# Kernel tuning notes

Measured on AMD Instinct MI355X. Metric: run time of the kernel, lower is better.

Reference implementation:

```python
import jax, jax.numpy as jnp
import numpy as np

C = 256
HEADS = 8
HD = C // HEADS
SCALE = HD ** -0.5


def conv1x1(x, W, b):
    # x: [B,C_in,H,W], W: [C_out,C_in], b: [C_out]
    return jnp.einsum('oc,bchw->bohw', W, x) + b[None, :, None, None]


def setup_inputs() -> dict:
    key = jax.random.key(0)
    ks = jax.random.split(key, 12)
    B, H, Wd = 2, 48, 48
    s = C ** -0.5
    return {
        'x': jax.random.normal(ks[0], (B, C, H, Wd), jnp.float32),
        'uncertainty': jax.random.uniform(ks[1], (B, 1, H, Wd), jnp.float32),
        'Wq': jax.random.normal(ks[2], (C, C), jnp.float32) * s,
        'bq': jnp.zeros((C,), jnp.float32),
        'Wk': jax.random.normal(ks[3], (C, C), jnp.float32) * s,
        'bk': jnp.zeros((C,), jnp.float32),
        'Wv': jax.random.normal(ks[4], (C, C), jnp.float32) * s,
        'bv': jnp.zeros((C,), jnp.float32),
        'Wg': jax.random.normal(ks[5], (C, 1), jnp.float32),
        'bg': jnp.zeros((C,), jnp.float32),
        'Wo': jax.random.normal(ks[6], (C, C), jnp.float32) * s,
        'bo': jnp.zeros((C,), jnp.float32),
    }


def reference(x, uncertainty, Wq, bq, Wk, bk, Wv, bv, Wg, bg, Wo, bo):
    B, _, H, Wd = x.shape
    N = H * Wd
    # uncertainty gate (1x1 conv from 1 channel to C channels)
    uw = conv1x1(uncertainty, Wg, bg)            # [B,C,H,W]
    gated_x = x * (1.0 - uw)
    q = conv1x1(gated_x, Wq, bq).reshape(B, HEADS, HD, N)
    k = conv1x1(gated_x, Wk, bk).reshape(B, HEADS, HD, N)
    v = conv1x1(x, Wv, bv).reshape(B, HEADS, HD, N)
    # scores: [B,h,N,N] (query tokens n, key tokens m)
    scores = jnp.einsum('bhdn,bhdm->bhnm', q, k) * SCALE
    u_flat = uncertainty.reshape(B, 1, 1, N)      # mask over key axis
    scores = scores * (1.0 - u_flat)
    attn = jax.nn.softmax(scores, axis=-1)
    out = jnp.einsum('bhnm,bhdm->bhdn', attn, v)  # [B,h,hd,N]
    out = out.reshape(B, C, H, Wd)
    out = conv1x1(out, Wo, bo)
    return out + x
```

## Files before the change

### kernel.cpp

```cpp
#include <hip/hip_runtime.h>
#include <hip/hip_bf16.h>

typedef float f32x4 __attribute__((ext_vector_type(4)));
typedef __bf16 bf16x8 __attribute__((ext_vector_type(8)));
typedef __bf16 bf16x4 __attribute__((ext_vector_type(4)));
typedef short s16x4 __attribute__((ext_vector_type(4)));

constexpr int C = 256;
constexpr int N = 2304;
constexpr int T = 2 * N;

#if __has_builtin(__builtin_amdgcn_exp2f)
#define EXP2F(x) __builtin_amdgcn_exp2f(x)
#else
#define EXP2F(x) exp2f(x)
#endif

__device__ __forceinline__ bf16x8 load_bf8(const __bf16* p) {
    return *reinterpret_cast<const bf16x8*>(p);
}

__device__ __forceinline__ f32x4 mfma32(bf16x8 a, bf16x8 b, f32x4 c) {
    return __builtin_amdgcn_mfma_f32_16x16x32_bf16(a, b, c, 0, 0, 0);
}

#if __has_builtin(__builtin_amdgcn_mfma_f32_16x16x16bf16_1k)
__device__ __forceinline__ f32x4 mfma16(bf16x4 a, bf16x4 b, f32x4 c) {
    return __builtin_amdgcn_mfma_f32_16x16x16bf16_1k(
        __builtin_bit_cast(s16x4, a), __builtin_bit_cast(s16x4, b), c, 0, 0, 0);
}
#else
__device__ __forceinline__ f32x4 mfma16(bf16x4 a, bf16x4 b, f32x4 c) {
    f32x4 d;
    asm volatile("v_mfma_f32_16x16x16_bf16 %0, %1, %2, %3"
                 : "=v"(d) : "v"(a), "v"(b), "v"(c));
    return d;
}
#endif

__device__ __forceinline__ void gload_lds16(const __bf16* g, __bf16* l) {
    __builtin_amdgcn_global_load_lds(
        (const __attribute__((address_space(1))) void*)g,
        (__attribute__((address_space(3))) void*)l, 16, 0, 0);
}

#define VMCNT2() asm volatile("s_waitcnt vmcnt(2)" ::: "memory")
#define VMCNT0() asm volatile("s_waitcnt vmcnt(0)" ::: "memory")
#define LGKM0()  asm volatile("s_waitcnt lgkmcnt(0)" ::: "memory")

__global__ void wconv_kernel(const float* __restrict__ Wq, const float* __restrict__ Wk,
                             const float* __restrict__ Wv, const float* __restrict__ Wo,
                             __bf16* __restrict__ Wb) {
    const float* srcs[4] = {Wq, Wk, Wv, Wo};
    int m = blockIdx.x >> 6;
    int idx = (blockIdx.x & 63) * 256 + threadIdx.x;
    float4 v = reinterpret_cast<const float4*>(srcs[m])[idx];
    bf16x4 o = { (__bf16)v.x, (__bf16)v.y, (__bf16)v.z, (__bf16)v.w };
    reinterpret_cast<bf16x4*>(Wb + m * 65536)[idx] = o;
}

__global__ void prep_kernel(const float* __restrict__ x, const float* __restrict__ u,
                            const float* __restrict__ Wg, const float* __restrict__ bg,
                            __bf16* __restrict__ xT, __bf16* __restrict__ gxT) {
    __shared__ float tile[64][65];
    int b = blockIdx.z, c0 = blockIdx.y * 64, n0 = blockIdx.x * 64;
    int t = threadIdx.x;
    const float* xp = x + (b * C + c0) * N + n0;
    #pragma unroll
    for (int r = 0; r < 16; ++r) {
        int cl = r * 4 + (t >> 6);
        int nl = t & 63;
        tile[cl][nl] = xp[cl * N + nl];
    }
    __syncthreads();
    int cq = (t & 15) * 4;
    #pragma unroll
    for (int it = 0; it < 4; ++it) {
        int nl = it * 16 + (t >> 4);
        float uv = u[b * N + n0 + nl];
        bf16x4 xo, go;
        #pragma unroll
        for (int j = 0; j < 4; ++j) {
            int c = c0 + cq + j;
            float xv = tile[cq + j][nl];
            float gate = 1.0f - (Wg[c] * uv + bg[c]);
            xo[j] = (__bf16)xv;
            go[j] = (__bf16)(xv * gate);
        }
        int tok = b * N + n0 + nl;
        *reinterpret_cast<bf16x4*>(xT + (long)tok * C + c0 + cq) = xo;
        *reinterpret_cast<bf16x4*>(gxT + (long)tok * C + c0 + cq) = go;
    }
}

__global__ __launch_bounds__(256) void qkv_kernel(const __bf16* __restrict__ Wb,
    const __bf16* __restrict__ xT, const __bf16* __restrict__ gxT,
    const float* __restrict__ bq, const float* __restrict__ bk, const float* __restrict__ bv,
    const float* __restrict__ u,
    __bf16* __restrict__ Q, __bf16* __restrict__ K, __bf16* __restrict__ V) {
    int proj = blockIdx.z;
    int o0 = blockIdx.y * 64;
    int t0 = blockIdx.x * 32;
    int wave = threadIdx.x >> 6, lane = threadIdx.x & 63;
    int g = lane >> 4, r = lane & 15;
    int ow = o0 + wave * 16;
    const __bf16* W = Wb + proj * 65536;
    const __bf16* inp = (proj == 2) ? xT : gxT;
    f32x4 acc[2] = {};
    for (int k = 0; k < 8; ++k) {
        bf16x8 a = load_bf8(W + (ow + r) * C + k * 32 + g * 8);
        #pragma unroll
        for (int tb = 0; tb < 2; ++tb) {
            bf16x8 bfr = load_bf8(inp + (long)(t0 + tb * 16 + r) * C + k * 32 + g * 8);
            acc[tb] = mfma32(a, bfr, acc[tb]);
        }
    }
    const float* bias = (proj == 0) ? bq : (proj == 1) ? bk : bv;
    float bvw[4];
    #pragma unroll
    for (int i = 0; i < 4; ++i) bvw[i] = bias[ow + g * 4 + i];
    int h = ow >> 5, d0 = (ow & 31) + g * 4;
    const float SC = 0.17677669529663687f * 1.4426950408889634f;
    #pragma unroll
    for (int tb = 0; tb < 2; ++tb) {
        int t = t0 + tb * 16 + r;
        int b = t / N, n = t % N;
        if (proj == 2) {
            #pragma unroll
            for (int i = 0; i < 4; ++i)
                V[((long)(b * 8 + h) * 32 + d0 + i) * N + n] = (__bf16)(acc[tb][i] + bvw[i]);
        } else {
            bf16x4 outv;
            if (proj == 1) {
                float scale = SC * (1.0f - u[t]);
                #pragma unroll
                for (int i = 0; i < 4; ++i) outv[i] = (__bf16)((acc[tb][i] + bvw[i]) * scale);
            } else {
                #pragma unroll
                for (int i = 0; i < 4; ++i) outv[i] = (__bf16)(acc[tb][i] + bvw[i]);
            }
            __bf16* dst = (proj == 0) ? Q : K;
            *reinterpret_cast<bf16x4*>(dst + ((long)(b * 8 + h) * N + n) * 32 + d0) = outv;
        }
    }
}

__global__ __launch_bounds__(256) void attn_kernel(const __bf16* __restrict__ Q,
    const __bf16* __restrict__ K, const __bf16* __restrict__ V,
    __bf16* __restrict__ aoT) {
    __shared__ __bf16 sK[2][2048];
    __shared__ __bf16 sV[2][2048];
    int id = blockIdx.x;
    int xcd = id & 7, j = id >> 3;
    int bh = xcd + 8 * (j / 36);
    int qblk = j % 36;
    int wave = threadIdx.x >> 6, lane = threadIdx.x & 63;
    int g = lane >> 4, r = lane & 15;
    int q0w = qblk * 64 + wave * 16;
    const __bf16* Qg = Q + (long)bh * N * 32;
    const __bf16* Kg = K + (long)bh * N * 32;
    const __bf16* Vg = V + (long)bh * 32 * N;
    bf16x8 qf = load_bf8(Qg + (q0w + r) * 32 + g * 8);
    long ksrc = (long)(wave * 64 + lane) * 8;
    int vd = wave * 8 + (lane >> 3);
    long vsrc = (long)vd * N + ((lane & 7) ^ (lane >> 3)) * 8;
    __bf16* sKb = &sK[0][0];
    __bf16* sVb = &sV[0][0];
    int sOff = wave * 512;
    bf16x4 onesv;
    #pragma unroll
    for (int i = 0; i < 4; ++i) onesv[i] = (__bf16)1.0f;
    f32x4 oa0 = {}, oa1 = {}, oal = {};
    gload_lds16(Kg + ksrc, sKb + sOff);
    gload_lds16(Vg + vsrc, sVb + sOff);
    gload_lds16(Kg + 64 * 32 + ksrc, sKb + 2048 + sOff);
    gload_lds16(Vg + vsrc + 64, sVb + 2048 + sOff);
    int vswz = (r & 7) << 3;
    for (int t = 0; t < 36; ++t) {
        if (t < 35) { VMCNT2(); } else { VMCNT0(); }
        __builtin_amdgcn_s_barrier();
        const __bf16* kb = sKb + (t & 1) * 2048;
        const __bf16* vb = sVb + (t & 1) * 2048;
        bf16x8 kc0 = load_bf8(kb + (0 * 16 + r) * 32 + g * 8);
        bf16x8 kc1 = load_bf8(kb + (1 * 16 + r) * 32 + g * 8);
        bf16x8 kc2 = load_bf8(kb + (2 * 16 + r) * 32 + g * 8);
        bf16x8 kc3 = load_bf8(kb + (3 * 16 + r) * 32 + g * 8);
        bf16x4 vf[4][2];
        #pragma unroll
        for (int tt = 0; tt < 4; ++tt)
            #pragma unroll
            for (int dt = 0; dt < 2; ++dt)
                vf[tt][dt] = *reinterpret_cast<const bf16x4*>(
                    vb + (dt * 16 + r) * 64 + ((tt * 16 + g * 4) ^ vswz));
        f32x4 z = {};
        __builtin_amdgcn_s_setprio(1);
        f32x4 s0 = mfma32(kc0, qf, z);
        f32x4 s1 = mfma32(kc1, qf, z);
        f32x4 s2 = mfma32(kc2, qf, z);
        f32x4 s3 = mfma32(kc3, qf, z);
        __builtin_amdgcn_s_setprio(0);
        bf16x4 pa0, pa1, pa2, pa3;
        #pragma unroll
        for (int i = 0; i < 4; ++i) pa0[i] = (__bf16)EXP2F(s0[i]);
        #pragma unroll
        for (int i = 0; i < 4; ++i) pa1[i] = (__bf16)EXP2F(s1[i]);
        #pragma unroll
        for (int i = 0; i < 4; ++i) pa2[i] = (__bf16)EXP2F(s2[i]);
        #pragma unroll
        for (int i = 0; i < 4; ++i) pa3[i] = (__bf16)EXP2F(s3[i]);
        __builtin_amdgcn_s_setprio(1);
        oa0 = mfma16(vf[0][0], pa0, oa0);
        oa1 = mfma16(vf[0][1], pa0, oa1);
        oal = mfma16(onesv,    pa0, oal);
        oa0 = mfma16(vf[1][0], pa1, oa0);
        oa1 = mfma16(vf[1][1], pa1, oa1);
        oal = mfma16(onesv,    pa1, oal);
        oa0 = mfma16(vf[2][0], pa2, oa0);
        oa1 = mfma16(vf[2][1], pa2, oa1);
        oal = mfma16(onesv,    pa2, oal);
        oa0 = mfma16(vf[3][0], pa3, oa0);
        oa1 = mfma16(vf[3][1], pa3, oa1);
        oal = mfma16(onesv,    pa3, oal);
        __builtin_amdgcn_s_setprio(0);
        LGKM0();
        __builtin_amdgcn_s_barrier();
        if (t < 34) {
            long m0n = (long)(t + 2) * 64;
            gload_lds16(Kg + m0n * 32 + ksrc, sKb + (t & 1) * 2048 + sOff);
            gload_lds16(Vg + vsrc + m0n, sVb + (t & 1) * 2048 + sOff);
        }
    }
    float inv = 1.0f / oal[0];
    int b = bh >> 3, h = bh & 7;
    long tok = (long)b * N + q0w + r;
    bf16x4 ov0, ov1;
    #pragma unroll
    for (int i = 0; i < 4; ++i) ov0[i] = (__bf16)(oa0[i] * inv);
    #pragma unroll
    for (int i = 0; i < 4; ++i) ov1[i] = (__bf16)(oa1[i] * inv);
    *reinterpret_cast<bf16x4*>(aoT + tok * C + h * 32 + g * 4) = ov0;
    *reinterpret_cast<bf16x4*>(aoT + tok * C + h * 32 + 16 + g * 4) = ov1;
}

__global__ __launch_bounds__(256) void outp_kernel(const __bf16* __restrict__ Wb,
    const __bf16* __restrict__ aoT, const float* __restrict__ bo,
    const float* __restrict__ x, float* __restrict__ out) {
    int o0 = blockIdx.y * 64;
    int t0 = blockIdx.x * 32;
    int wave = threadIdx.x >> 6, lane = threadIdx.x & 63;
    int g = lane >> 4, r = lane & 15;
    int ow = o0 + wave * 16;
    const __bf16* W = Wb + 3 * 65536;
    f32x4 acc[2] = {};
    for (int k = 0; k < 8; ++k) {
        bf16x8 a = load_bf8(W + (ow + r) * C + k * 32 + g * 8);
        #pragma unroll
        for (int tb = 0; tb < 2; ++tb) {
            bf16x8 bfr = load_bf8(aoT + (long)(t0 + tb * 16 + r) * C + k * 32 + g * 8);
            acc[tb] = mfma32(a, bfr, acc[tb]);
        }
    }
    float bvw[4];
    #pragma unroll
    for (int i = 0; i < 4; ++i) bvw[i] = bo[ow + g * 4 + i];
    #pragma unroll
    for (int tb = 0; tb < 2; ++tb) {
        int t = t0 + tb * 16 + r;
        int b = t / N, n = t % N;
        #pragma unroll
        for (int i = 0; i < 4; ++i) {
            long idx = ((long)b * C + ow + g * 4 + i) * N + n;
            out[idx] = acc[tb][i] + bvw[i] + x[idx];
        }
    }
}

extern "C" void kernel_launch(void* const* d_in, const int* in_sizes, int n_in,
                              void* d_out, int out_size, void* d_ws, size_t ws_size,
                              hipStream_t stream) {
    const float* x  = (const float*)d_in[0];
    const float* u  = (const float*)d_in[1];
    const float* Wq = (const float*)d_in[2];
    const float* bq = (const float*)d_in[3];
    const float* Wk = (const float*)d_in[4];
    const float* bk = (const float*)d_in[5];
    const float* Wv = (const float*)d_in[6];
    const float* bv = (const float*)d_in[7];
    const float* Wg = (const float*)d_in[8];
    const float* bg = (const float*)d_in[9];
    const float* Wo = (const float*)d_in[10];
    const float* bo = (const float*)d_in[11];
    float* out = (float*)d_out;

    char* ws = (char*)d_ws;
    size_t off = 0;
    auto alloc = [&](size_t bytes) {
        char* p = ws + off;
        off += (bytes + 255) & ~(size_t)255;
        return p;
    };
    __bf16* Wb  = (__bf16*)alloc((size_t)4 * 65536 * 2);
    __bf16* xT  = (__bf16*)alloc((size_t)T * C * 2);
    __bf16* gxT = (__bf16*)alloc((size_t)T * C * 2);
    __bf16* Qb  = (__bf16*)alloc((size_t)16 * N * 32 * 2);
    __bf16* Kb  = (__bf16*)alloc((size_t)16 * N * 32 * 2);
    __bf16* Vb  = (__bf16*)alloc((size_t)16 * N * 32 * 2);
    __bf16* aoT = (__bf16*)alloc((size_t)T * C * 2);

    wconv_kernel<<<256, 256, 0, stream>>>(Wq, Wk, Wv, Wo, Wb);
    prep_kernel<<<dim3(36, 4, 2), 256, 0, stream>>>(x, u, Wg, bg, xT, gxT);
    qkv_kernel<<<dim3(144, 4, 3), 256, 0, stream>>>(Wb, xT, gxT, bq, bk, bv, u, Qb, Kb, Vb);
    attn_kernel<<<576, 256, 0, stream>>>(Qb, Kb, Vb, aoT);
    outp_kernel<<<dim3(144, 4), 256, 0, stream>>>(Wb, aoT, bo, x, out);
}
```

Measured before the change: 81.15 us.

## Triple-buffer attention K/V staging and halve block size to 128 threads

```diff
diff --git a/kernel.cpp b/kernel.cpp
--- a/kernel.cpp
+++ b/kernel.cpp
@@ -44,7 +44,7 @@
         (__attribute__((address_space(3))) void*)l, 16, 0, 0);
 }
 
-#define VMCNT2() asm volatile("s_waitcnt vmcnt(2)" ::: "memory")
+#define VMCNT4() asm volatile("s_waitcnt vmcnt(4)" ::: "memory")
 #define VMCNT0() asm volatile("s_waitcnt vmcnt(0)" ::: "memory")
 #define LGKM0()  asm volatile("s_waitcnt lgkmcnt(0)" ::: "memory")
 
@@ -145,53 +145,61 @@
     }
 }
 
-__global__ __launch_bounds__(256) void attn_kernel(const __bf16* __restrict__ Q,
+__global__ __launch_bounds__(128) void attn_kernel(const __bf16* __restrict__ Q,
     const __bf16* __restrict__ K, const __bf16* __restrict__ V,
     __bf16* __restrict__ aoT) {
-    __shared__ __bf16 sK[2][2048];
-    __shared__ __bf16 sV[2][2048];
+    __shared__ __bf16 sK[3][2048];
+    __shared__ __bf16 sV[3][2048];
     int id = blockIdx.x;
     int xcd = id & 7, j = id >> 3;
-    int bh = xcd + 8 * (j / 36);
-    int qblk = j % 36;
-    int wave = threadIdx.x >> 6, lane = threadIdx.x & 63;
+    int bh = xcd + 8 * (j / 72);
+    int qblk = j % 72;
+    int tid = threadIdx.x;
+    int wave = tid >> 6, lane = tid & 63;
     int g = lane >> 4, r = lane & 15;
-    int q0w = qblk * 64 + wave * 16;
+    int q0w = qblk * 32 + wave * 16;
     const __bf16* Qg = Q + (long)bh * N * 32;
     const __bf16* Kg = K + (long)bh * N * 32;
     const __bf16* Vg = V + (long)bh * 32 * N;
     bf16x8 qf = load_bf8(Qg + (q0w + r) * 32 + g * 8);
-    long ksrc = (long)(wave * 64 + lane) * 8;
-    int vd = wave * 8 + (lane >> 3);
-    long vsrc = (long)vd * N + ((lane & 7) ^ (lane >> 3)) * 8;
-    __bf16* sKb = &sK[0][0];
-    __bf16* sVb = &sV[0][0];
-    int sOff = wave * 512;
+    long ka = (long)tid * 8;
+    int rrA = tid >> 3;
+    int clA = (tid & 7) ^ ((tid >> 4) & 7);
+    long va = (long)rrA * N + clA * 8;
+    int so = wave * 512;
+    auto STAGE = [&](long m0, __bf16* kd, __bf16* vd) {
+        gload_lds16(Kg + m0 * 32 + ka,          kd + so);
+        gload_lds16(Kg + m0 * 32 + 1024 + ka,   kd + 1024 + so);
+        gload_lds16(Vg + va + m0,               vd + so);
+        gload_lds16(Vg + va + 16 * N + m0,      vd + 1024 + so);
+    };
+    __bf16 *kA = &sK[0][0], *kB = &sK[1][0], *kC = &sK[2][0];
+    __bf16 *vA = &sV[0][0], *vB = &sV[1][0], *vC = &sV[2][0];
     bf16x4 onesv;
     #pragma unroll
     for (int i = 0; i < 4; ++i) onesv[i] = (__bf16)1.0f;
     f32x4 oa0 = {}, oa1 = {}, oal = {};
-    gload_lds16(Kg + ksrc, sKb + sOff);
-    gload_lds16(Vg + vsrc, sVb + sOff);
-    gload_lds16(Kg + 64 * 32 + ksrc, sKb + 2048 + sOff);
-    gload_lds16(Vg + vsrc + 64, sVb + 2048 + sOff);
-    int vswz = (r & 7) << 3;
+    STAGE(0, kA, vA);
+    STAGE(64, kB, vB);
+    int k2r = (r >> 1) & 7;
     for (int t = 0; t < 36; ++t) {
-        if (t < 35) { VMCNT2(); } else { VMCNT0(); }
+        LGKM0();
+        if (t < 34) { VMCNT4(); } else { VMCNT0(); }
         __builtin_amdgcn_s_barrier();
-        const __bf16* kb = sKb + (t & 1) * 2048;
-        const __bf16* vb = sVb + (t & 1) * 2048;
-        bf16x8 kc0 = load_bf8(kb + (0 * 16 + r) * 32 + g * 8);
-        bf16x8 kc1 = load_bf8(kb + (1 * 16 + r) * 32 + g * 8);
-        bf16x8 kc2 = load_bf8(kb + (2 * 16 + r) * 32 + g * 8);
-        bf16x8 kc3 = load_bf8(kb + (3 * 16 + r) * 32 + g * 8);
+        if (t < 34) STAGE((long)(t + 2) * 64, kC, vC);
+        bf16x8 kc0 = load_bf8(kA + (0 * 16 + r) * 32 + g * 8);
+        bf16x8 kc1 = load_bf8(kA + (1 * 16 + r) * 32 + g * 8);
+        bf16x8 kc2 = load_bf8(kA + (2 * 16 + r) * 32 + g * 8);
+        bf16x8 kc3 = load_bf8(kA + (3 * 16 + r) * 32 + g * 8);
         bf16x4 vf[4][2];
         #pragma unroll
-        for (int tt = 0; tt < 4; ++tt)
+        for (int tt = 0; tt < 4; ++tt) {
+            int pg = (((tt * 2 + (g >> 1)) ^ k2r) << 1) | (g & 1);
             #pragma unroll
             for (int dt = 0; dt < 2; ++dt)
                 vf[tt][dt] = *reinterpret_cast<const bf16x4*>(
-                    vb + (dt * 16 + r) * 64 + ((tt * 16 + g * 4) ^ vswz));
+                    vA + (dt * 16 + r) * 64 + pg * 4);
+        }
         f32x4 z = {};
         __builtin_amdgcn_s_setprio(1);
         f32x4 s0 = mfma32(kc0, qf, z);
@@ -222,13 +230,8 @@
         oa1 = mfma16(vf[3][1], pa3, oa1);
         oal = mfma16(onesv,    pa3, oal);
         __builtin_amdgcn_s_setprio(0);
-        LGKM0();
-        __builtin_amdgcn_s_barrier();
-        if (t < 34) {
-            long m0n = (long)(t + 2) * 64;
-            gload_lds16(Kg + m0n * 32 + ksrc, sKb + (t & 1) * 2048 + sOff);
-            gload_lds16(Vg + vsrc + m0n, sVb + (t & 1) * 2048 + sOff);
-        }
+        __bf16* tk = kA; kA = kB; kB = kC; kC = tk;
+        __bf16* tv = vA; vA = vB; vB = vC; vC = tv;
     }
     float inv = 1.0f / oal[0];
     int b = bh >> 3, h = bh & 7;
@@ -310,6 +313,6 @@
     wconv_kernel<<<256, 256, 0, stream>>>(Wq, Wk, Wv, Wo, Wb);
     prep_kernel<<<dim3(36, 4, 2), 256, 0, stream>>>(x, u, Wg, bg, xT, gxT);
     qkv_kernel<<<dim3(144, 4, 3), 256, 0, stream>>>(Wb, xT, gxT, bq, bk, bv, u, Qb, Kb, Vb);
-    attn_kernel<<<576, 256, 0, stream>>>(Qb, Kb, Vb, aoT);
+    attn_kernel<<<1152, 128, 0, stream>>>(Qb, Kb, Vb, aoT);
     outp_kernel<<<dim3(144, 4), 256, 0, stream>>>(Wb, aoT, bo, x, out);
 }
```

Measured after the change: 78.97 us. 1.03x faster.
